# Optimization experiments

Hardware: AMD Instinct MI355X
Metric: run time of the kernel (lower is better)

Reference implementation:

```python
import jax, jax.numpy as jnp
import numpy as np

B, D, C = 4096, 256, 64  # batch, dim_embed, n_conditions
EPS = 1e-10


def setup_inputs() -> dict:
    key = jax.random.key(0)
    k1, k2, k3, k4 = jax.random.split(key, 4)
    x = jax.random.normal(k1, (B, D), dtype=jnp.float32)          # embedded_x (embeddingnet = identity)
    W = jax.random.normal(k2, (C, D, D), dtype=jnp.float32) * 0.02  # per-condition Linear weights (out,in)
    b = jax.random.normal(k3, (C, D), dtype=jnp.float32) * 0.02     # per-condition Linear biases
    c = jax.random.randint(k4, (B,), 0, C)                         # condition index per sample
    return {"x": x, "W": W, "b": b, "c": c}


def reference(x, W, b, c):
    # per-sample expert Linear: y_i = W[c_i] @ x_i + b[c_i]
    y = jnp.einsum('bij,bj->bi', W[c], x) + b[c]          # [B, D]
    # mask_norm accumulates L1 norm of the selected weight PER SAMPLE (duplicates counted)
    per_cond_l1 = jnp.sum(jnp.abs(W), axis=(1, 2))        # [C]
    mask_norm = jnp.sum(per_cond_l1[c])
    # embed_norm = global L2 (Frobenius) norm of embedded_x
    embed_norm = jnp.sqrt(jnp.sum(x * x))
    # F.normalize(p=2, dim=1, eps=1e-10): divide by max(row_norm, eps)
    row_norm = jnp.sqrt(jnp.sum(y * y, axis=1, keepdims=True))
    masked_embedding = y / jnp.maximum(row_norm, EPS)
    return (masked_embedding, mask_norm, embed_norm, x)
```

## Files before the change

kernel.cpp:

```cpp
#include <hip/hip_runtime.h>
#include <math.h>

#define B_ 4096
#define D_ 256
#define C_ 64
#define BD (B_*D_)

typedef __attribute__((ext_vector_type(8))) short bf16x8;
typedef __attribute__((ext_vector_type(4))) float f32x4;

__device__ __forceinline__ float wave_reduce_sum(float v) {
    #pragma unroll
    for (int off = 1; off < 64; off <<= 1) v += __shfl_xor(v, off);
    return v;
}

__device__ __forceinline__ unsigned cvtpk(float lo, float hi) {
    unsigned r;
    asm volatile("v_cvt_pk_bf16_f32 %0, %1, %2" : "=v"(r) : "v"(lo), "v"(hi));
    return r;
}

__global__ __launch_bounds__(256, 2) void k_main(const float* __restrict__ W,
                                                 const float* __restrict__ b,
                                                 const float* __restrict__ x,
                                                 const int* __restrict__ c,
                                                 float* __restrict__ out,
                                                 float* __restrict__ l1p,
                                                 float* __restrict__ xsqp,
                                                 int* __restrict__ cnt4) {
    int hw = blockIdx.x;
    int bid = (hw & 7) * 64 + (hw >> 3);
    int cond = bid >> 3;
    int ct = (bid >> 2) & 1;
    int sl = bid & 3;
    int tid = threadIdx.x;
    int wv = tid >> 6, lane = tid & 63;
    int g = lane >> 4, fr = lane & 15;
    int wr = tid >> 1, wh = tid & 1;

    const float4* x4 = (const float4*)x;
    float4 xv0 = x4[bid * 512 + tid];
    float4 xv1 = x4[bid * 512 + 256 + tid];
    int4 cvq[4];
    #pragma unroll
    for (int t = 0; t < 4; ++t) cvq[t] = ((const int4*)c)[t * 256 + tid];
    const float4* Wt4 = (const float4*)(W + (size_t)cond * 65536) + (size_t)(ct * 128 + wr) * 64 + wh * 4;
    float4 wA[4], wB[4];
    #pragma unroll
    for (int j = 0; j < 4; ++j) wA[j] = Wt4[j];
    float bias0 = b[cond * 256 + ct * 128 + wv * 32 + fr];
    float bias1 = b[cond * 256 + ct * 128 + wv * 32 + 16 + fr];

    __shared__ unsigned Xl[48 * 128];
    __shared__ unsigned Wl[2][128 * 20];
    __shared__ float part_x[4];
    __shared__ float part_w[4];
    __shared__ int slist[48];
    __shared__ int nlist;
    if (tid == 0) nlist = 0;

    float2* dst = (float2*)(out + BD + 2);
    int xi = bid * 512 + tid;
    dst[2 * xi]             = make_float2(xv0.x, xv0.y);
    dst[2 * xi + 1]         = make_float2(xv0.z, xv0.w);
    dst[2 * (xi + 256)]     = make_float2(xv1.x, xv1.y);
    dst[2 * (xi + 256) + 1] = make_float2(xv1.z, xv1.w);
    float s = xv0.x * xv0.x + xv0.y * xv0.y + xv0.z * xv0.z + xv0.w * xv0.w
            + xv1.x * xv1.x + xv1.y * xv1.y + xv1.z * xv1.z + xv1.w * xv1.w;
    s = wave_reduce_sum(s);
    if (lane == 0) part_x[wv] = s;
    __syncthreads();

    #pragma unroll
    for (int t = 0; t < 4; ++t) {
        int4 q = cvq[t];
        int cc = (sl == 0) ? q.x : (sl == 1) ? q.y : (sl == 2) ? q.z : q.w;
        if (cc == cond) {
            int p = atomicAdd(&nlist, 1);
            if (p < 48) slist[p] = 4 * (t * 256 + tid) + sl;
        }
    }
    #pragma unroll
    for (int j = 0; j < 4; ++j)
        asm volatile("" : "+v"(wA[j].x), "+v"(wA[j].y), "+v"(wA[j].z), "+v"(wA[j].w));
    __syncthreads();
    int n = min(nlist, 48);
    int mts = (n + 15) >> 4;
    if (tid == 0) {
        xsqp[bid] = (part_x[0] + part_x[1]) + (part_x[2] + part_x[3]);
        if (ct == 0) cnt4[cond * 4 + sl] = n;
    }

    int sgr[12];
    #pragma unroll
    for (int k = 0; k < 12; ++k) sgr[k] = slist[wv + 4 * k];
    #pragma unroll
    for (int k = 0; k < 12; ++k) {
        int u = tid + 256 * k;
        if (u < n * 64) {
            int si = u >> 6, v = u & 63;
            float4 q = x4[(size_t)sgr[k] * 64 + v];
            int off = (v * 8) ^ ((si & 7) << 4);
            Xl[si * 128 + (off >> 2)]     = cvtpk(q.x, q.y);
            Xl[si * 128 + (off >> 2) + 1] = cvtpk(q.z, q.w);
        }
    }

    float l1acc = 0.f;
    {
        uint4 pk;
        pk.x = cvtpk(wA[0].x, wA[0].y); pk.y = cvtpk(wA[0].z, wA[0].w);
        pk.z = cvtpk(wA[1].x, wA[1].y); pk.w = cvtpk(wA[1].z, wA[1].w);
        *(uint4*)(&Wl[0][wr * 20 + wh * 8]) = pk;
        pk.x = cvtpk(wA[2].x, wA[2].y); pk.y = cvtpk(wA[2].z, wA[2].w);
        pk.z = cvtpk(wA[3].x, wA[3].y); pk.w = cvtpk(wA[3].z, wA[3].w);
        *(uint4*)(&Wl[0][wr * 20 + wh * 8 + 4]) = pk;
        if (sl == 0) {
            #pragma unroll
            for (int j = 0; j < 4; ++j)
                l1acc += fabsf(wA[j].x) + fabsf(wA[j].y) + fabsf(wA[j].z) + fabsf(wA[j].w);
        }
    }
    #pragma unroll
    for (int j = 0; j < 4; ++j) wB[j] = Wt4[8 + j];
    __syncthreads();

    f32x4 acc[3][2];
    #pragma unroll
    for (int mt = 0; mt < 3; ++mt) {
        acc[mt][0] = (f32x4){0.f, 0.f, 0.f, 0.f};
        acc[mt][1] = (f32x4){0.f, 0.f, 0.f, 0.f};
    }

    #pragma unroll
    for (int kk = 0; kk < 8; ++kk) {
        const unsigned* Wb = Wl[kk & 1];
        bf16x8 bfr0 = *(const bf16x8*)(Wb + (wv * 32 + fr) * 20 + g * 4);
        bf16x8 bfr1 = *(const bf16x8*)(Wb + (wv * 32 + 16 + fr) * 20 + g * 4);
        #pragma unroll
        for (int mt = 0; mt < 3; ++mt) if (mt < mts) {
            int row = mt * 16 + fr;
            bf16x8 afr = *(const bf16x8*)((const char*)Xl + row * 512 + ((kk * 64 + g * 16) ^ ((row & 7) << 4)));
            acc[mt][0] = __builtin_amdgcn_mfma_f32_16x16x32_bf16(afr, bfr0, acc[mt][0], 0, 0, 0);
            acc[mt][1] = __builtin_amdgcn_mfma_f32_16x16x32_bf16(afr, bfr1, acc[mt][1], 0, 0, 0);
        }
        if (kk < 7) {
            const float4* wsrc = (kk & 1) ? wA : wB;
            unsigned* wdst = &Wl[(kk + 1) & 1][wr * 20 + wh * 8];
            uint4 pk;
            pk.x = cvtpk(wsrc[0].x, wsrc[0].y); pk.y = cvtpk(wsrc[0].z, wsrc[0].w);
            pk.z = cvtpk(wsrc[1].x, wsrc[1].y); pk.w = cvtpk(wsrc[1].z, wsrc[1].w);
            *(uint4*)(wdst) = pk;
            pk.x = cvtpk(wsrc[2].x, wsrc[2].y); pk.y = cvtpk(wsrc[2].z, wsrc[2].w);
            pk.z = cvtpk(wsrc[3].x, wsrc[3].y); pk.w = cvtpk(wsrc[3].z, wsrc[3].w);
            *(uint4*)(wdst + 4) = pk;
            if (sl == 0) {
                #pragma unroll
                for (int j = 0; j < 4; ++j)
                    l1acc += fabsf(wsrc[j].x) + fabsf(wsrc[j].y) + fabsf(wsrc[j].z) + fabsf(wsrc[j].w);
            }
            if (kk < 6) {
                float4* wld = (kk & 1) ? wB : wA;
                #pragma unroll
                for (int j = 0; j < 4; ++j) wld[j] = Wt4[(kk + 2) * 8 + j];
            }
            __syncthreads();
        }
    }

    if (sl == 0) {
        float a = wave_reduce_sum(l1acc);
        if (lane == 0) part_w[wv] = a;
    }
    __syncthreads();
    if (sl == 0 && tid == 0)
        l1p[cond * 2 + ct] = (part_w[0] + part_w[1]) + (part_w[2] + part_w[3]);

    #pragma unroll
    for (int mt = 0; mt < 3; ++mt) if (mt < mts) {
        #pragma unroll
        for (int j = 0; j < 4; ++j) {
            int row = mt * 16 + g * 4 + j;
            if (row < n) {
                int sg = slist[row];
                float* op = out + (size_t)sg * 256 + ct * 128 + wv * 32 + fr;
                op[0]  = acc[mt][0][j] + bias0;
                op[16] = acc[mt][1][j] + bias1;
            }
        }
    }
}

__global__ __launch_bounds__(256) void k_fin(float* __restrict__ out,
                                             const float* __restrict__ xsqp,
                                             const float* __restrict__ l1p,
                                             const int* __restrict__ cnt4) {
    int tid = threadIdx.x;
    int wv = tid >> 6, lane = tid & 63;
    if (blockIdx.x == 1024) {
        __shared__ float part[4];
        float s = xsqp[tid] + xsqp[tid + 256];
        s = wave_reduce_sum(s);
        if (lane == 0) part[wv] = s;
        __syncthreads();
        if (tid < 64) {
            float l1 = l1p[tid * 2] + l1p[tid * 2 + 1];
            float cnt = (float)((cnt4[tid * 4 + 0] + cnt4[tid * 4 + 1]) + (cnt4[tid * 4 + 2] + cnt4[tid * 4 + 3]));
            float mv = l1 * cnt;
            mv = wave_reduce_sum(mv);
            if (tid == 0) out[BD] = mv;
        }
        if (tid == 0) out[BD + 1] = sqrtf((part[0] + part[1]) + (part[2] + part[3]));
        return;
    }
    int rowv = blockIdx.x * 4 + wv;
    float4* p = (float4*)out + (size_t)rowv * 64 + lane;
    float4 v = *p;
    float s = v.x * v.x + v.y * v.y + v.z * v.z + v.w * v.w;
    s = wave_reduce_sum(s);
    float inv = 1.0f / fmaxf(sqrtf(s), 1e-10f);
    v.x *= inv; v.y *= inv; v.z *= inv; v.w *= inv;
    *p = v;
}

extern "C" void kernel_launch(void* const* d_in, const int* in_sizes, int n_in,
                              void* d_out, int out_size, void* d_ws, size_t ws_size,
                              hipStream_t stream) {
    const float* x = (const float*)d_in[0];
    const float* W = (const float*)d_in[1];
    const float* b = (const float*)d_in[2];
    const int*   c = (const int*)d_in[3];
    float* out = (float*)d_out;

    float* xsqp = (float*)d_ws;
    float* l1p  = xsqp + 512;
    int*   cnt4 = (int*)(l1p + 128);

    k_main<<<512, 256, 0, stream>>>(W, b, x, c, out, l1p, xsqp, cnt4);
    k_fin<<<1025, 256, 0, stream>>>(out, xsqp, l1p, cnt4);
}
```

Measured before the change: 19.31 us.

## Split each condition's output columns into four tiles across twice as many blocks

```diff
diff --git a/kernel.cpp b/kernel.cpp
--- a/kernel.cpp
+++ b/kernel.cpp
@@ -21,7 +21,7 @@
     return r;
 }
 
-__global__ __launch_bounds__(256, 2) void k_main(const float* __restrict__ W,
+__global__ __launch_bounds__(256, 4) void k_main(const float* __restrict__ W,
                                                  const float* __restrict__ b,
                                                  const float* __restrict__ x,
                                                  const int* __restrict__ c,
@@ -30,30 +30,28 @@
                                                  float* __restrict__ xsqp,
                                                  int* __restrict__ cnt4) {
     int hw = blockIdx.x;
-    int bid = (hw & 7) * 64 + (hw >> 3);
-    int cond = bid >> 3;
-    int ct = (bid >> 2) & 1;
+    int bid = (hw & 7) * 128 + (hw >> 3);
+    int cond = bid >> 4;
+    int ct = (bid >> 2) & 3;
     int sl = bid & 3;
     int tid = threadIdx.x;
     int wv = tid >> 6, lane = tid & 63;
     int g = lane >> 4, fr = lane & 15;
-    int wr = tid >> 1, wh = tid & 1;
+    int r = tid >> 2, ch = tid & 3;
 
     const float4* x4 = (const float4*)x;
-    float4 xv0 = x4[bid * 512 + tid];
-    float4 xv1 = x4[bid * 512 + 256 + tid];
+    int xi = bid * 256 + tid;
+    float4 xv = x4[xi];
     int4 cvq[4];
     #pragma unroll
     for (int t = 0; t < 4; ++t) cvq[t] = ((const int4*)c)[t * 256 + tid];
-    const float4* Wt4 = (const float4*)(W + (size_t)cond * 65536) + (size_t)(ct * 128 + wr) * 64 + wh * 4;
-    float4 wA[4], wB[4];
-    #pragma unroll
-    for (int j = 0; j < 4; ++j) wA[j] = Wt4[j];
-    float bias0 = b[cond * 256 + ct * 128 + wv * 32 + fr];
-    float bias1 = b[cond * 256 + ct * 128 + wv * 32 + 16 + fr];
+    const float4* Wt4 = (const float4*)(W + (size_t)cond * 65536) + (size_t)(ct * 64 + r) * 64 + ch * 2;
+    float4 wA[2], wB[2];
+    wA[0] = Wt4[0]; wA[1] = Wt4[1];
+    float bias_s = b[cond * 256 + ct * 64 + wv * 16 + fr];
 
     __shared__ unsigned Xl[48 * 128];
-    __shared__ unsigned Wl[2][128 * 20];
+    __shared__ unsigned Wl[2][64 * 20];
     __shared__ float part_x[4];
     __shared__ float part_w[4];
     __shared__ int slist[48];
@@ -61,13 +59,9 @@
     if (tid == 0) nlist = 0;
 
     float2* dst = (float2*)(out + BD + 2);
-    int xi = bid * 512 + tid;
-    dst[2 * xi]             = make_float2(xv0.x, xv0.y);
-    dst[2 * xi + 1]         = make_float2(xv0.z, xv0.w);
-    dst[2 * (xi + 256)]     = make_float2(xv1.x, xv1.y);
-    dst[2 * (xi + 256) + 1] = make_float2(xv1.z, xv1.w);
-    float s = xv0.x * xv0.x + xv0.y * xv0.y + xv0.z * xv0.z + xv0.w * xv0.w
-            + xv1.x * xv1.x + xv1.y * xv1.y + xv1.z * xv1.z + xv1.w * xv1.w;
+    dst[2 * xi]     = make_float2(xv.x, xv.y);
+    dst[2 * xi + 1] = make_float2(xv.z, xv.w);
+    float s = xv.x * xv.x + xv.y * xv.y + xv.z * xv.z + xv.w * xv.w;
     s = wave_reduce_sum(s);
     if (lane == 0) part_x[wv] = s;
     __syncthreads();
@@ -81,9 +75,8 @@
             if (p < 48) slist[p] = 4 * (t * 256 + tid) + sl;
         }
     }
-    #pragma unroll
-    for (int j = 0; j < 4; ++j)
-        asm volatile("" : "+v"(wA[j].x), "+v"(wA[j].y), "+v"(wA[j].z), "+v"(wA[j].w));
+    asm volatile("" : "+v"(wA[0].x), "+v"(wA[0].y), "+v"(wA[0].z), "+v"(wA[0].w),
+                      "+v"(wA[1].x), "+v"(wA[1].y), "+v"(wA[1].z), "+v"(wA[1].w));
     __syncthreads();
     int n = min(nlist, 48);
     int mts = (n + 15) >> 4;
@@ -112,58 +105,41 @@
         uint4 pk;
         pk.x = cvtpk(wA[0].x, wA[0].y); pk.y = cvtpk(wA[0].z, wA[0].w);
         pk.z = cvtpk(wA[1].x, wA[1].y); pk.w = cvtpk(wA[1].z, wA[1].w);
-        *(uint4*)(&Wl[0][wr * 20 + wh * 8]) = pk;
-        pk.x = cvtpk(wA[2].x, wA[2].y); pk.y = cvtpk(wA[2].z, wA[2].w);
-        pk.z = cvtpk(wA[3].x, wA[3].y); pk.w = cvtpk(wA[3].z, wA[3].w);
-        *(uint4*)(&Wl[0][wr * 20 + wh * 8 + 4]) = pk;
-        if (sl == 0) {
-            #pragma unroll
-            for (int j = 0; j < 4; ++j)
-                l1acc += fabsf(wA[j].x) + fabsf(wA[j].y) + fabsf(wA[j].z) + fabsf(wA[j].w);
-        }
-    }
-    #pragma unroll
-    for (int j = 0; j < 4; ++j) wB[j] = Wt4[8 + j];
-    __syncthreads();
-
-    f32x4 acc[3][2];
-    #pragma unroll
-    for (int mt = 0; mt < 3; ++mt) {
-        acc[mt][0] = (f32x4){0.f, 0.f, 0.f, 0.f};
-        acc[mt][1] = (f32x4){0.f, 0.f, 0.f, 0.f};
-    }
+        *(uint4*)(&Wl[0][r * 20 + ch * 4]) = pk;
+        if (sl == 0)
+            l1acc += fabsf(wA[0].x) + fabsf(wA[0].y) + fabsf(wA[0].z) + fabsf(wA[0].w)
+                   + fabsf(wA[1].x) + fabsf(wA[1].y) + fabsf(wA[1].z) + fabsf(wA[1].w);
+    }
+    wB[0] = Wt4[8]; wB[1] = Wt4[9];
+    __syncthreads();
+
+    f32x4 acc[3];
+    #pragma unroll
+    for (int mt = 0; mt < 3; ++mt) acc[mt] = (f32x4){0.f, 0.f, 0.f, 0.f};
 
     #pragma unroll
     for (int kk = 0; kk < 8; ++kk) {
         const unsigned* Wb = Wl[kk & 1];
-        bf16x8 bfr0 = *(const bf16x8*)(Wb + (wv * 32 + fr) * 20 + g * 4);
-        bf16x8 bfr1 = *(const bf16x8*)(Wb + (wv * 32 + 16 + fr) * 20 + g * 4);
+        bf16x8 bfr = *(const bf16x8*)(Wb + (wv * 16 + fr) * 20 + g * 4);
         #pragma unroll
         for (int mt = 0; mt < 3; ++mt) if (mt < mts) {
             int row = mt * 16 + fr;
             bf16x8 afr = *(const bf16x8*)((const char*)Xl + row * 512 + ((kk * 64 + g * 16) ^ ((row & 7) << 4)));
-            acc[mt][0] = __builtin_amdgcn_mfma_f32_16x16x32_bf16(afr, bfr0, acc[mt][0], 0, 0, 0);
-            acc[mt][1] = __builtin_amdgcn_mfma_f32_16x16x32_bf16(afr, bfr1, acc[mt][1], 0, 0, 0);
+            acc[mt] = __builtin_amdgcn_mfma_f32_16x16x32_bf16(afr, bfr, acc[mt], 0, 0, 0);
         }
         if (kk < 7) {
             const float4* wsrc = (kk & 1) ? wA : wB;
-            unsigned* wdst = &Wl[(kk + 1) & 1][wr * 20 + wh * 8];
             uint4 pk;
             pk.x = cvtpk(wsrc[0].x, wsrc[0].y); pk.y = cvtpk(wsrc[0].z, wsrc[0].w);
             pk.z = cvtpk(wsrc[1].x, wsrc[1].y); pk.w = cvtpk(wsrc[1].z, wsrc[1].w);
-            *(uint4*)(wdst) = pk;
-            pk.x = cvtpk(wsrc[2].x, wsrc[2].y); pk.y = cvtpk(wsrc[2].z, wsrc[2].w);
-            pk.z = cvtpk(wsrc[3].x, wsrc[3].y); pk.w = cvtpk(wsrc[3].z, wsrc[3].w);
-            *(uint4*)(wdst + 4) = pk;
-            if (sl == 0) {
-                #pragma unroll
-                for (int j = 0; j < 4; ++j)
-                    l1acc += fabsf(wsrc[j].x) + fabsf(wsrc[j].y) + fabsf(wsrc[j].z) + fabsf(wsrc[j].w);
-            }
+            *(uint4*)(&Wl[(kk + 1) & 1][r * 20 + ch * 4]) = pk;
+            if (sl == 0)
+                l1acc += fabsf(wsrc[0].x) + fabsf(wsrc[0].y) + fabsf(wsrc[0].z) + fabsf(wsrc[0].w)
+                       + fabsf(wsrc[1].x) + fabsf(wsrc[1].y) + fabsf(wsrc[1].z) + fabsf(wsrc[1].w);
             if (kk < 6) {
                 float4* wld = (kk & 1) ? wB : wA;
-                #pragma unroll
-                for (int j = 0; j < 4; ++j) wld[j] = Wt4[(kk + 2) * 8 + j];
+                wld[0] = Wt4[(kk + 2) * 8];
+                wld[1] = Wt4[(kk + 2) * 8 + 1];
             }
             __syncthreads();
         }
@@ -175,7 +151,7 @@
     }
     __syncthreads();
     if (sl == 0 && tid == 0)
-        l1p[cond * 2 + ct] = (part_w[0] + part_w[1]) + (part_w[2] + part_w[3]);
+        l1p[cond * 4 + ct] = (part_w[0] + part_w[1]) + (part_w[2] + part_w[3]);
 
     #pragma unroll
     for (int mt = 0; mt < 3; ++mt) if (mt < mts) {
@@ -184,9 +160,7 @@
             int row = mt * 16 + g * 4 + j;
             if (row < n) {
                 int sg = slist[row];
-                float* op = out + (size_t)sg * 256 + ct * 128 + wv * 32 + fr;
-                op[0]  = acc[mt][0][j] + bias0;
-                op[16] = acc[mt][1][j] + bias1;
+                out[(size_t)sg * 256 + ct * 64 + wv * 16 + fr] = acc[mt][j] + bias_s;
             }
         }
     }
@@ -200,12 +174,14 @@
     int wv = tid >> 6, lane = tid & 63;
     if (blockIdx.x == 1024) {
         __shared__ float part[4];
-        float s = xsqp[tid] + xsqp[tid + 256];
+        float s = 0.f;
+        #pragma unroll
+        for (int j = 0; j < 4; ++j) s += xsqp[tid * 4 + j];
         s = wave_reduce_sum(s);
         if (lane == 0) part[wv] = s;
         __syncthreads();
         if (tid < 64) {
-            float l1 = l1p[tid * 2] + l1p[tid * 2 + 1];
+            float l1 = (l1p[tid * 4 + 0] + l1p[tid * 4 + 1]) + (l1p[tid * 4 + 2] + l1p[tid * 4 + 3]);
             float cnt = (float)((cnt4[tid * 4 + 0] + cnt4[tid * 4 + 1]) + (cnt4[tid * 4 + 2] + cnt4[tid * 4 + 3]));
             float mv = l1 * cnt;
             mv = wave_reduce_sum(mv);
@@ -234,9 +210,9 @@
     float* out = (float*)d_out;
 
     float* xsqp = (float*)d_ws;
-    float* l1p  = xsqp + 512;
-    int*   cnt4 = (int*)(l1p + 128);
-
-    k_main<<<512, 256, 0, stream>>>(W, b, x, c, out, l1p, xsqp, cnt4);
+    float* l1p  = xsqp + 1024;
+    int*   cnt4 = (int*)(l1p + 256);
+
+    k_main<<<1024, 256, 0, stream>>>(W, b, x, c, out, l1p, xsqp, cnt4);
     k_fin<<<1025, 256, 0, stream>>>(out, xsqp, l1p, cnt4);
 }
```

Measured after the change: 18.40 us (median of 2 runs). 1.05x faster.
